# Optimization experiments

Hardware: AMD Instinct MI355X
Metric: run time of the kernel (lower is better)

The kernel has to match this reference:

```python
import jax, jax.numpy as jnp
import numpy as np

D_MODEL = 512
D_EMB = 300
D_FIXED = 30000
D_EXT = 32000
BS, L, J, N, T = 8, 256, 48, 32, 48


def setup_inputs() -> dict:
    key = jax.random.key(0)
    ks = jax.random.split(key, 32)
    s = 0.02
    def nrm(k, shape, scale=0.02):
        return jax.random.normal(k, shape, dtype=jnp.float32) * scale
    inp = {
        "Mp": jax.random.normal(ks[0], (BS, L, D_MODEL), dtype=jnp.float32),
        "Mq": jax.random.normal(ks[1], (BS, J, D_MODEL), dtype=jnp.float32),
        "Mqa": jax.random.normal(ks[2], (BS, N, D_MODEL), dtype=jnp.float32),
        "Mnlg": jax.random.normal(ks[3], (BS, T, D_MODEL), dtype=jnp.float32),
        "mask_p": jnp.ones((BS, L, 1), dtype=bool),
        "mask_q": jnp.ones((BS, J, 1), dtype=bool),
        "mask_qa": jnp.ones((BS, N, 1), dtype=bool),
        "source_ext": jax.random.randint(ks[4], (BS, L + J + N), 0, D_EXT, dtype=jnp.int64) if jax.config.jax_enable_x64 else jax.random.randint(ks[4], (BS, L + J + N), 0, D_EXT).astype(jnp.int32),
        "special_mask": jnp.ones((D_FIXED,), dtype=bool).at[jnp.array([0, 1, 2, 3])].set(False),
        "d_ext_vocab": D_EXT,
    }
    # additive attention params for question / qa / passage branches
    names = ["q", "a", "p"]
    for i, nme in enumerate(names):
        base = 5 + 5 * i
        inp[f"Wk_{nme}"] = nrm(ks[base + 0], (D_MODEL, D_MODEL))
        inp[f"bk_{nme}"] = jnp.zeros((D_MODEL,), dtype=jnp.float32)
        inp[f"Wq_{nme}"] = nrm(ks[base + 1], (D_MODEL, D_MODEL))
        inp[f"bq_{nme}"] = jnp.zeros((D_MODEL,), dtype=jnp.float32)
        inp[f"v_{nme}"] = nrm(ks[base + 2], (D_MODEL,))
    # vocab generator: Linear(d_model, d_emb) -> Linear(d_emb, d_fixed, bias=False)
    inp["W1"] = nrm(ks[20], (D_MODEL, D_EMB))
    inp["b1"] = jnp.zeros((D_EMB,), dtype=jnp.float32)
    inp["W2"] = nrm(ks[21], (D_EMB, D_FIXED))
    # mixture: Linear(4*d_model, 4) + softmax
    inp["Wm"] = nrm(ks[22], (4 * D_MODEL, 4))
    inp["bm"] = jnp.zeros((4,), dtype=jnp.float32)
    return inp


def _additive_attn(K, V, Q, mask, Wk, bk, Wq, bq, v):
    # K,V: [b,S,d]; Q: [b,T,d]; mask: [b,S,1] bool
    Kp = K @ Wk + bk                                  # [b,S,d]
    Qp = Q @ Wq + bq                                  # [b,T,d]
    scores = jnp.einsum("btsd,d->bts", jnp.tanh(Qp[:, :, None, :] + Kp[:, None, :, :]), v)
    scores = jnp.where(mask[:, None, :, 0], scores, -1e9)
    attn = jax.nn.softmax(scores, axis=-1)            # [b,T,S]
    ctx = jnp.einsum("bts,bsd->btd", attn, V)         # [b,T,d]
    return ctx, attn


def reference(Mp, Mq, Mqa, Mnlg, mask_p, mask_q, mask_qa, source_ext, special_mask,
              Wk_q, bk_q, Wq_q, bq_q, v_q,
              Wk_a, bk_a, Wq_a, bq_a, v_a,
              Wk_p, bk_p, Wq_p, bq_p, v_p,
              W1, b1, W2, Wm, bm, d_ext_vocab):
    d_fixed = special_mask.shape[0]
    bs, Tq, _ = Mnlg.shape

    ctx_q, q_distr = _additive_attn(Mq, Mq, Mnlg, mask_q, Wk_q, bk_q, Wq_q, bq_q, v_q)
    ctx_a, qa_distr = _additive_attn(Mqa, Mqa, Mnlg, mask_qa, Wk_a, bk_a, Wq_a, bq_a, v_a)
    ctx_p, p_distr = _additive_attn(Mp, Mp, Mnlg, mask_p, Wk_p, bk_p, Wq_p, bq_p, v_p)

    # fixed-vocab distribution with special tokens masked out
    logits = (Mnlg @ W1 + b1) @ W2                    # [b,T,d_fixed]
    logits = jnp.where(special_mask[None, None, :], logits, -1e9)
    fixed_vocab_distr = jax.nn.softmax(logits, axis=-1)

    # mixture weights
    mix_in = jnp.concatenate([Mnlg, ctx_q, ctx_a, ctx_p], axis=-1)  # [b,T,4d]
    lambdas = jax.nn.softmax(mix_in @ Wm + bm, axis=-1)             # [b,T,4]
    lam_v, lam_q, lam_qa, lam_p = jnp.split(lambdas, 4, axis=-1)

    fixed_vocab_distr = fixed_vocab_distr * lam_v
    source_distr = jnp.concatenate([p_distr * lam_p, q_distr * lam_q, qa_distr * lam_qa], axis=-1)  # [b,T,S_tot]

    # scatter-add over extended vocab (math-equivalent to one_hot + matmul)
    def _scatter(src, idx):
        # src: [T,S_tot], idx: [S_tot]
        return jnp.zeros((Tq, d_ext_vocab), src.dtype).at[:, idx].add(src)

    ext_vocab_distr = jax.vmap(_scatter)(source_distr, source_ext)  # [b,T,d_ext]
    ext_vocab_distr = ext_vocab_distr.at[:, :, :d_fixed].add(fixed_vocab_distr)
    return ext_vocab_distr, lambdas
```

## Files before the change

### kernel.cpp

```cpp
#include <hip/hip_runtime.h>
#include <math.h>

#define BS     8
#define LL     256
#define JJ     48
#define NN     32
#define TT     48
#define DM     512
#define DEMB   300
#define DFIX   30000
#define DEXT   32000
#define SRC_TOT (LL + JJ + NN)
#define ROWS   (BS * TT)
#define NT     235
#define KH     320

typedef float f32x4  __attribute__((ext_vector_type(4)));
typedef short bf16x8 __attribute__((ext_vector_type(8)));

__device__ __forceinline__ short f2bf(float f) {
    union { float f; unsigned u; } v; v.f = f;
    return (short)((v.u + 0x7FFFu + ((v.u >> 16) & 1u)) >> 16);
}
__device__ __forceinline__ float bf2f(short s) {
    union { unsigned u; float f; } v;
    v.u = ((unsigned)(unsigned short)s) << 16;
    return v.f;
}
__device__ __forceinline__ float fast_exp2(float x) {
#if __has_builtin(__builtin_amdgcn_exp2f)
    return __builtin_amdgcn_exp2f(x);
#else
    return exp2f(x);
#endif
}
__device__ __forceinline__ float fast_rcp(float x) {
#if __has_builtin(__builtin_amdgcn_rcpf)
    return __builtin_amdgcn_rcpf(x);
#else
    return 1.f / x;
#endif
}
__device__ __forceinline__ float fast_tanh(float x) {
    x = fminf(fmaxf(x, -15.f), 15.f);
    const float e = fast_exp2(x * 2.885390082f);
    return (e - 1.f) * fast_rcp(e + 1.f);
}
__device__ __forceinline__ bool smask_true(const void* smask, bool byteLayout, int i)
{
    if (byteLayout) return ((const unsigned char*)smask)[i] != 0;
    return ((const int*)smask)[i] != 0;
}
__device__ __forceinline__ void mask8(const void* smask, bool byteLayout, int i,
                                      int* mb)
{
    if (byteLayout) {
        const uchar4 a = ((const uchar4*)((const unsigned char*)smask + i))[0];
        const uchar4 b = ((const uchar4*)((const unsigned char*)smask + i))[1];
        mb[0]=a.x; mb[1]=a.y; mb[2]=a.z; mb[3]=a.w;
        mb[4]=b.x; mb[5]=b.y; mb[6]=b.z; mb[7]=b.w;
    } else {
        const int* p = (const int*)smask + i;
        #pragma unroll
        for (int j = 0; j < 8; ++j) mb[j] = p[j];
    }
}

struct PDesc { const float* src; short* dst; int K, N, Kp, ntx, tiles; };
struct PArgs { PDesc d[12]; int nd; };

__global__ __launch_bounds__(256) void prep_kernel(PArgs pa)
{
    __shared__ short T[64][72];
    int tile = blockIdx.x, g = 0;
    while (g + 1 < pa.nd && tile >= pa.d[g].tiles) { tile -= pa.d[g].tiles; ++g; }
    const PDesc d = pa.d[g];
    const int tid = threadIdx.x;

    if (d.ntx == 0) {
        const int i = (tile * 256 + tid) * 8;
        if (i < d.K) {
            const float4 a = ((const float4*)(d.src + i))[0];
            const float4 b = ((const float4*)(d.src + i))[1];
            bf16x8 v;
            v[0]=f2bf(a.x); v[1]=f2bf(a.y); v[2]=f2bf(a.z); v[3]=f2bf(a.w);
            v[4]=f2bf(b.x); v[5]=f2bf(b.y); v[6]=f2bf(b.z); v[7]=f2bf(b.w);
            *(bf16x8*)&d.dst[i] = v;
        }
        return;
    }

    const int kt = tile / d.ntx, nt = tile % d.ntx;
    const int k0 = kt * 64, n0 = nt * 64;
    {
        const int n = n0 + (tid & 63);
        #pragma unroll
        for (int p = 0; p < 16; ++p) {
            const int kk = p * 4 + (tid >> 6);
            const int k = k0 + kk;
            float v = 0.f;
            if (k < d.K && n < d.N) v = d.src[(size_t)k * d.N + n];
            T[kk][tid & 63] = f2bf(v);
        }
    }
    __syncthreads();
    {
        const int nn = tid >> 2;
        const int kq = (tid & 3) * 16;
        const int n = n0 + nn;
        if (n < d.N) {
            bf16x8 v0, v1;
            #pragma unroll
            for (int j = 0; j < 8; ++j) v0[j] = T[kq + j][nn];
            #pragma unroll
            for (int j = 0; j < 8; ++j) v1[j] = T[kq + 8 + j][nn];
            *(bf16x8*)&d.dst[(size_t)n * d.Kp + k0 + kq]     = v0;
            *(bf16x8*)&d.dst[(size_t)n * d.Kp + k0 + kq + 8] = v1;
        }
    }
}

struct GDesc { const short* A; const short* Bt; const float* bias; void* C;
               const void* smask; float* pstat;
               int M, N, K, Kp, nx, my, obf, npad, nt, tiles; };
struct GArgs { GDesc d[7]; int nd; };

__global__ __launch_bounds__(256) void gemm_bf16_kernel(GArgs ga)
{
    __shared__ short As[2][4][130][8];
    __shared__ short Bs[2][4][130][8];
    __shared__ float pm_s[128][2];
    __shared__ float ps_s[128][2];

    int tile = blockIdx.x, g = 0;
    while (g + 1 < ga.nd && tile >= ga.d[g].tiles) { tile -= ga.d[g].tiles; ++g; }
    const short* __restrict__ A  = ga.d[g].A;
    const short* __restrict__ Bt = ga.d[g].Bt;
    const float* bias = ga.d[g].bias;
    const int N = ga.d[g].N, Kp = ga.d[g].Kp;
    const int nx = ga.d[g].nx, my = ga.d[g].my, obf = ga.d[g].obf;
    const int npad = ga.d[g].npad;

    int bm, bn;
    if (my > 0) { bm = (tile % my) * 128; bn = (tile / my) * 128; }
    else        { bm = (tile / nx) * 128; bn = (tile % nx) * 128; }
    const int tid  = threadIdx.x;
    const int lane = tid & 63;
    const int wv   = tid >> 6;
    const int wm   = (wv >> 1) * 64;
    const int wn   = (wv & 1) * 64;

    bf16x8 ra[2], rb[2];

    auto loadA = [&](int k0) {
        #pragma unroll
        for (int p = 0; p < 2; ++p) {
            const int row = p * 64 + (tid >> 2);
            ra[p] = *(const bf16x8*)&A[(size_t)(bm + row) * Kp + k0 + (tid & 3) * 8];
        }
    };
    auto loadB = [&](int k0) {
        #pragma unroll
        for (int p = 0; p < 2; ++p) {
            const int idx = p * 256 + tid;
            const int n = idx >> 2, kb = idx & 3;
            const int gn = bn + n;
            bf16x8 v = {};
            if (gn < N) v = *(const bf16x8*)&Bt[(size_t)gn * Kp + k0 + kb * 8];
            rb[p] = v;
        }
    };
    auto storeA = [&](int buf) {
        const int kb = tid & 3;
        #pragma unroll
        for (int p = 0; p < 2; ++p)
            *(bf16x8*)&As[buf][kb][p * 64 + (tid >> 2)][0] = ra[p];
    };
    auto storeB = [&](int buf) {
        #pragma unroll
        for (int p = 0; p < 2; ++p) {
            const int idx = p * 256 + tid;
            const int n = idx >> 2, kb = idx & 3;
            *(bf16x8*)&Bs[buf][kb][n][0] = rb[p];
        }
    };

    f32x4 acc[4][4] = {};
    const int nk = Kp / 32;

    loadA(0); loadB(0);
    storeA(0); storeB(0);
    __syncthreads();

    for (int kk = 0; kk < nk; ++kk) {
        const int cur = kk & 1;
        if (kk + 1 < nk) { loadA((kk + 1) * 32); loadB((kk + 1) * 32); }
        bf16x8 af[4], bfr[4];
        #pragma unroll
        for (int i = 0; i < 4; ++i) {
            af[i]  = *(const bf16x8*)&As[cur][lane >> 4][wm + i * 16 + (lane & 15)][0];
            bfr[i] = *(const bf16x8*)&Bs[cur][lane >> 4][wn + i * 16 + (lane & 15)][0];
        }
        #pragma unroll
        for (int mi = 0; mi < 4; ++mi)
            #pragma unroll
            for (int ni = 0; ni < 4; ++ni)
                acc[mi][ni] = __builtin_amdgcn_mfma_f32_16x16x32_bf16(
                    af[mi], bfr[ni], acc[mi][ni], 0, 0, 0);
        if (kk + 1 < nk) { storeA(cur ^ 1); storeB(cur ^ 1); }
        __syncthreads();
    }

    if (obf == 0) {
        float* Cf = (float*)ga.d[g].C;
        #pragma unroll
        for (int ni = 0; ni < 4; ++ni) {
            const int gn = bn + wn + ni * 16 + (lane & 15);
            if (gn >= N) continue;
            const float bb = bias ? bias[gn] : 0.f;
            #pragma unroll
            for (int mi = 0; mi < 4; ++mi)
                #pragma unroll
                for (int r = 0; r < 4; ++r) {
                    const int gm = bm + wm + mi * 16 + (lane >> 4) * 4 + r;
                    Cf[(size_t)gm * N + gn] = acc[mi][ni][r] + bb;
                }
        }
    } else if (obf == 2) {
        short* Cs = (short*)ga.d[g].C;
        #pragma unroll
        for (int ni = 0; ni < 4; ++ni) {
            const int gn = bn + wn + ni * 16 + (lane & 15);
            if (gn >= npad) continue;
            const bool valid = (gn < N);
            const float bb = (valid && bias) ? bias[gn] : 0.f;
            #pragma unroll
            for (int mi = 0; mi < 4; ++mi)
                #pragma unroll
                for (int r = 0; r < 4; ++r) {
                    const int gm = bm + wm + mi * 16 + (lane >> 4) * 4 + r;
                    Cs[(size_t)gm * npad + gn] = valid ? f2bf(acc[mi][ni][r] + bb) : (short)0;
                }
        }
    } else {
        short* Cs = (short*)ga.d[g].C;
        const void* sm = ga.d[g].smask;
        const bool byteLayout = (((const int*)sm)[1] == 0x01010101);
        int mk[4];
        #pragma unroll
        for (int ni = 0; ni < 4; ++ni) {
            const int gn = bn + wn + ni * 16 + (lane & 15);
            const bool inb = (gn < N);
            mk[ni] = inb && smask_true(sm, byteLayout, inb ? gn : 0);
            if (inb) {
                #pragma unroll
                for (int mi = 0; mi < 4; ++mi)
                    #pragma unroll
                    for (int r = 0; r < 4; ++r) {
                        const int gm = bm + wm + mi * 16 + (lane >> 4) * 4 + r;
                        Cs[(size_t)gm * N + gn] = f2bf(acc[mi][ni][r]);
                    }
            }
        }
        #pragma unroll
        for (int mi = 0; mi < 4; ++mi) {
            #pragma unroll
            for (int r = 0; r < 4; ++r) {
                const int rl = wm + mi * 16 + (lane >> 4) * 4 + r;
                float vmax = -INFINITY;
                #pragma unroll
                for (int ni = 0; ni < 4; ++ni)
                    if (mk[ni]) vmax = fmaxf(vmax, acc[mi][ni][r]);
                #pragma unroll
                for (int o = 1; o < 16; o <<= 1)
                    vmax = fmaxf(vmax, __shfl_xor(vmax, o));
                float se = 0.f;
                #pragma unroll
                for (int ni = 0; ni < 4; ++ni)
                    if (mk[ni]) se += __expf(acc[mi][ni][r] - vmax);
                #pragma unroll
                for (int o = 1; o < 16; o <<= 1)
                    se += __shfl_xor(se, o);
                if ((lane & 15) == 0) {
                    pm_s[rl][wn >> 6] = vmax;
                    ps_s[rl][wn >> 6] = se;
                }
            }
        }
        __syncthreads();
        if (tid < 128) {
            const float mA = pm_s[tid][0], mB = pm_s[tid][1];
            const float sA = ps_s[tid][0], sB = ps_s[tid][1];
            const float m = fmaxf(mA, mB);
            float s = 0.f;
            if (sA > 0.f) s += sA * __expf(mA - m);
            if (sB > 0.f) s += sB * __expf(mB - m);
            float* ps = ga.d[g].pstat;
            const size_t idx = ((size_t)(bm + tid) * ga.d[g].nt + (bn >> 7)) * 2;
            ps[idx + 0] = m;
            ps[idx + 1] = s;
        }
    }
}

struct SDesc { const float* Kp; const float* Qp; const float* vv;
               int Sb, s0, cnt, off; };
struct SArgs { SDesc c[6]; };

__global__ __launch_bounds__(256) void scores_kernel(SArgs sa,
                                                     float* __restrict__ scb)
{
    const SDesc d = sa.c[blockIdx.y];
    const int bt   = blockIdx.x;
    const int b    = bt / TT;
    const int tid  = threadIdx.x;
    const int lane = tid & 63;
    const int wave = tid >> 6;

    float qp[8], vv[8];
    {
        const float4* q4 = (const float4*)(d.Qp + (size_t)bt * DM) + lane * 2;
        float4 a = q4[0], c = q4[1];
        qp[0]=a.x; qp[1]=a.y; qp[2]=a.z; qp[3]=a.w;
        qp[4]=c.x; qp[5]=c.y; qp[6]=c.z; qp[7]=c.w;
        const float4* v4 = (const float4*)d.vv + lane * 2;
        a = v4[0]; c = v4[1];
        vv[0]=a.x; vv[1]=a.y; vv[2]=a.z; vv[3]=a.w;
        vv[4]=c.x; vv[5]=c.y; vv[6]=c.z; vv[7]=c.w;
    }
    for (int s = wave; s < d.cnt; s += 4) {
        const float* krow = d.Kp + ((size_t)b * d.Sb + d.s0 + s) * DM + lane * 8;
        const float4 ka = ((const float4*)krow)[0];
        const float4 kb = ((const float4*)krow)[1];
        float acc = 0.f;
        acc = fmaf(vv[0], fast_tanh(qp[0] + ka.x), acc);
        acc = fmaf(vv[1], fast_tanh(qp[1] + ka.y), acc);
        acc = fmaf(vv[2], fast_tanh(qp[2] + ka.z), acc);
        acc = fmaf(vv[3], fast_tanh(qp[3] + ka.w), acc);
        acc = fmaf(vv[4], fast_tanh(qp[4] + kb.x), acc);
        acc = fmaf(vv[5], fast_tanh(qp[5] + kb.y), acc);
        acc = fmaf(vv[6], fast_tanh(qp[6] + kb.z), acc);
        acc = fmaf(vv[7], fast_tanh(qp[7] + kb.w), acc);
        #pragma unroll
        for (int off = 32; off; off >>= 1) acc += __shfl_xor(acc, off);
        if (lane == 0) scb[(size_t)bt * SRC_TOT + d.off + s] = acc;
    }
}

__global__ __launch_bounds__(512) void attn2mix_kernel(
    const float* __restrict__ scb,
    const short* __restrict__ Mqb, const short* __restrict__ Mqab,
    const short* __restrict__ Mpb, const float* __restrict__ Mnlg,
    const float* __restrict__ Wm, const float* __restrict__ bm,
    const float* __restrict__ pstat,
    float* __restrict__ dQ, float* __restrict__ dQA, float* __restrict__ dP,
    float* __restrict__ lam_ws, float* __restrict__ lam_out,
    float* __restrict__ stat)
{
    __shared__ float a_sh[SRC_TOT];
    __shared__ float cQ[DM], cA[DM], cP[DM];
    __shared__ float red[16];
    __shared__ float redm[32];
    __shared__ float s_lamv;
    const int bt   = blockIdx.x;
    const int b    = bt / TT;
    const int tid  = threadIdx.x;
    const int lane = tid & 63;
    const int wave = tid >> 6;
    const float* srow = scb + (size_t)bt * SRC_TOT;

    #pragma unroll
    for (int br = 0; br < 3; ++br) {
        const int off = (br == 0) ? 0 : (br == 1) ? JJ : (JJ + NN);
        const int cnt = (br == 0) ? JJ : (br == 1) ? NN : LL;
        float x = (tid < cnt) ? srow[off + tid] : -INFINITY;
        float m = x;
        #pragma unroll
        for (int o = 32; o; o >>= 1) m = fmaxf(m, __shfl_xor(m, o));
        if (lane == 0) red[wave] = m;
        __syncthreads();
        m = red[0];
        #pragma unroll
        for (int w = 1; w < 8; ++w) m = fmaxf(m, red[w]);
        float e = (tid < cnt) ? __expf(x - m) : 0.f;
        float ss = e;
        #pragma unroll
        for (int o = 32; o; o >>= 1) ss += __shfl_xor(ss, o);
        if (lane == 0) red[8 + wave] = ss;
        __syncthreads();
        float denom = 0.f;
        #pragma unroll
        for (int w = 0; w < 8; ++w) denom += red[8 + w];
        if (tid < cnt) {
            const float a = e / denom;
            a_sh[off + tid] = a;
            float* dst = (br == 0) ? dQ : (br == 1) ? dQA : dP;
            dst[(size_t)bt * cnt + tid] = a;
        }
        __syncthreads();
    }
    {
        float aQ = 0.f, aA = 0.f, aP = 0.f;
        for (int s = 0; s < JJ; ++s)
            aQ = fmaf(a_sh[s],           bf2f(Mqb [((size_t)b * JJ + s) * DM + tid]), aQ);
        for (int s = 0; s < NN; ++s)
            aA = fmaf(a_sh[JJ + s],      bf2f(Mqab[((size_t)b * NN + s) * DM + tid]), aA);
        for (int s = 0; s < LL; ++s)
            aP = fmaf(a_sh[JJ + NN + s], bf2f(Mpb [((size_t)b * LL + s) * DM + tid]), aP);
        cQ[tid] = aQ; cA[tid] = aA; cP[tid] = aP;
    }
    __syncthreads();
    {
        const float x0 = Mnlg[(size_t)bt * DM + tid];
        const float x1 = cQ[tid], x2 = cA[tid], x3 = cP[tid];
        const float4 w0 = *(const float4*)&Wm[(size_t)tid * 4];
        const float4 w1 = *(const float4*)&Wm[(size_t)(512 + tid) * 4];
        const float4 w2 = *(const float4*)&Wm[(size_t)(1024 + tid) * 4];
        const float4 w3 = *(const float4*)&Wm[(size_t)(1536 + tid) * 4];
        float acc[4];
        acc[0] = x0 * w0.x + x1 * w1.x + x2 * w2.x + x3 * w3.x;
        acc[1] = x0 * w0.y + x1 * w1.y + x2 * w2.y + x3 * w3.y;
        acc[2] = x0 * w0.z + x1 * w1.z + x2 * w2.z + x3 * w3.z;
        acc[3] = x0 * w0.w + x1 * w1.w + x2 * w2.w + x3 * w3.w;
        #pragma unroll
        for (int c = 0; c < 4; ++c)
            #pragma unroll
            for (int o = 32; o; o >>= 1) acc[c] += __shfl_xor(acc[c], o);
        if (lane == 0) {
            redm[wave * 4 + 0] = acc[0]; redm[wave * 4 + 1] = acc[1];
            redm[wave * 4 + 2] = acc[2]; redm[wave * 4 + 3] = acc[3];
        }
        __syncthreads();
        if (tid == 0) {
            float l[4];
            #pragma unroll
            for (int c = 0; c < 4; ++c) {
                float s = bm[c];
                #pragma unroll
                for (int w = 0; w < 8; ++w) s += redm[w * 4 + c];
                l[c] = s;
            }
            const float mx = fmaxf(fmaxf(l[0], l[1]), fmaxf(l[2], l[3]));
            const float e0 = __expf(l[0] - mx), e1 = __expf(l[1] - mx);
            const float e2 = __expf(l[2] - mx), e3 = __expf(l[3] - mx);
            const float inv = 1.f / (e0 + e1 + e2 + e3);
            s_lamv = e0 * inv;
            lam_ws[bt * 4 + 0] = e0 * inv; lam_out[bt * 4 + 0] = e0 * inv;
            lam_ws[bt * 4 + 1] = e1 * inv; lam_out[bt * 4 + 1] = e1 * inv;
            lam_ws[bt * 4 + 2] = e2 * inv; lam_out[bt * 4 + 2] = e2 * inv;
            lam_ws[bt * 4 + 3] = e3 * inv; lam_out[bt * 4 + 3] = e3 * inv;
        }
    }
    __syncthreads();
    if (wave == 0) {
        float m = -INFINITY;
        for (int c = lane; c < NT; c += 64)
            m = fmaxf(m, pstat[((size_t)bt * NT + c) * 2]);
        #pragma unroll
        for (int o = 32; o; o >>= 1) m = fmaxf(m, __shfl_xor(m, o));
        float s = 0.f;
        for (int c = lane; c < NT; c += 64) {
            const float pm = pstat[((size_t)bt * NT + c) * 2];
            const float ps = pstat[((size_t)bt * NT + c) * 2 + 1];
            if (ps > 0.f) s += ps * __expf(pm - m);
        }
        #pragma unroll
        for (int o = 32; o; o >>= 1) s += __shfl_xor(s, o);
        if (lane == 0) {
            stat[bt * 2 + 0] = m;
            stat[bt * 2 + 1] = s_lamv / s;
        }
    }
}

__global__ __launch_bounds__(1024) void writescatter_kernel(
    const short* __restrict__ logits, const void* __restrict__ smask,
    const float* __restrict__ stat, const float* __restrict__ lam,
    const float* __restrict__ dP, const float* __restrict__ dQ,
    const float* __restrict__ dQA, const void* __restrict__ src_ext,
    float* __restrict__ out)
{
    const bool byteLayout = (((const int*)smask)[1] == 0x01010101);
    const int r = blockIdx.x;
    const float m   = stat[r * 2 + 0];
    const float inv = stat[r * 2 + 1];

    const short* lrow = logits + (size_t)r * DFIX;
    float* orow = out + (size_t)r * DEXT;
    const int tid = threadIdx.x;
    #pragma unroll
    for (int k = 0; k < 4; ++k) {
        const int i = (k * 1024 + tid) * 8;
        if (i >= DEXT) continue;
        float4 o0 = make_float4(0.f, 0.f, 0.f, 0.f);
        float4 o1 = make_float4(0.f, 0.f, 0.f, 0.f);
        if (i < DFIX) {
            const bf16x8 v = *(const bf16x8*)&lrow[i];
            int mb[8]; mask8(smask, byteLayout, i, mb);
            o0.x = mb[0] ? __expf(bf2f(v[0]) - m) * inv : 0.f;
            o0.y = mb[1] ? __expf(bf2f(v[1]) - m) * inv : 0.f;
            o0.z = mb[2] ? __expf(bf2f(v[2]) - m) * inv : 0.f;
            o0.w = mb[3] ? __expf(bf2f(v[3]) - m) * inv : 0.f;
            o1.x = mb[4] ? __expf(bf2f(v[4]) - m) * inv : 0.f;
            o1.y = mb[5] ? __expf(bf2f(v[5]) - m) * inv : 0.f;
            o1.z = mb[6] ? __expf(bf2f(v[6]) - m) * inv : 0.f;
            o1.w = mb[7] ? __expf(bf2f(v[7]) - m) * inv : 0.f;
        }
        *(float4*)&orow[i]     = o0;
        *(float4*)&orow[i + 4] = o1;
    }
    __syncthreads();
    if (tid < SRC_TOT) {
        const int* s32 = (const int*)src_ext;
        const bool src64 = (s32[1] == 0 && s32[3] == 0 && s32[5] == 0 && s32[7] == 0);
        const int b = r / TT;
        const float lamq  = lam[r * 4 + 1];
        const float lamqa = lam[r * 4 + 2];
        const float lamp  = lam[r * 4 + 3];
        const int pos = b * SRC_TOT + tid;
        const int idx = src64 ? (int)((const long long*)src_ext)[pos] : s32[pos];
        float val;
        if      (tid < LL)      val = dP [(size_t)r * LL + tid]             * lamp;
        else if (tid < LL + JJ) val = dQ [(size_t)r * JJ + (tid - LL)]      * lamq;
        else                    val = dQA[(size_t)r * NN + (tid - LL - JJ)] * lamqa;
        atomicAdd(&orow[idx], val);
    }
}

extern "C" void kernel_launch(void* const* d_in, const int* in_sizes, int n_in,
                              void* d_out, int out_size, void* d_ws, size_t ws_size,
                              hipStream_t stream)
{
    const float* Mp   = (const float*)d_in[0];
    const float* Mq   = (const float*)d_in[1];
    const float* Mqa  = (const float*)d_in[2];
    const float* Mnlg = (const float*)d_in[3];
    const void* src_ext = d_in[7];
    const void* smask   = d_in[8];
    const float* Wk_q = (const float*)d_in[10];
    const float* bk_q = (const float*)d_in[11];
    const float* Wq_q = (const float*)d_in[12];
    const float* bq_q = (const float*)d_in[13];
    const float* v_q  = (const float*)d_in[14];
    const float* Wk_a = (const float*)d_in[15];
    const float* bk_a = (const float*)d_in[16];
    const float* Wq_a = (const float*)d_in[17];
    const float* bq_a = (const float*)d_in[18];
    const float* v_a  = (const float*)d_in[19];
    const float* Wk_p = (const float*)d_in[20];
    const float* bk_p = (const float*)d_in[21];
    const float* Wq_p = (const float*)d_in[22];
    const float* bq_p = (const float*)d_in[23];
    const float* v_p  = (const float*)d_in[24];
    const float* W1   = (const float*)d_in[25];
    const float* b1   = (const float*)d_in[26];
    const float* W2   = (const float*)d_in[27];
    const float* Wm   = (const float*)d_in[28];
    const float* bm   = (const float*)d_in[29];
    float* out = (float*)d_out;

    char* ws = (char*)d_ws;
    size_t off = 0;
    auto alloc = [&](size_t bytes) -> char* {
        char* p = ws + off;
        off += (bytes + 255) & ~(size_t)255;
        return p;
    };
    short* logits = (short*)alloc((size_t)ROWS * DFIX * 2);
    float* KpP    = (float*)alloc((size_t)BS * LL * DM * 4);
    float* KpQ    = (float*)alloc((size_t)BS * JJ * DM * 4);
    float* KpA    = (float*)alloc((size_t)BS * NN * DM * 4);
    float* QpQ    = (float*)alloc((size_t)ROWS * DM * 4);
    float* QpA    = (float*)alloc((size_t)ROWS * DM * 4);
    float* QpP    = (float*)alloc((size_t)ROWS * DM * 4);
    float* dP     = (float*)alloc((size_t)ROWS * LL * 4);
    float* dQ     = (float*)alloc((size_t)ROWS * JJ * 4);
    float* dQA    = (float*)alloc((size_t)ROWS * NN * 4);
    float* lam    = (float*)alloc((size_t)ROWS * 4 * 4);
    float* pstat  = (float*)alloc((size_t)ROWS * NT * 2 * 4);
    float* stat   = (float*)alloc((size_t)ROWS * 2 * 4);
    float* scb    = (float*)alloc((size_t)ROWS * SRC_TOT * 4);
    short* tWkq = (short*)alloc((size_t)DM * DM * 2);
    short* tWqq = (short*)alloc((size_t)DM * DM * 2);
    short* tWka = (short*)alloc((size_t)DM * DM * 2);
    short* tWqa = (short*)alloc((size_t)DM * DM * 2);
    short* tWkp = (short*)alloc((size_t)DM * DM * 2);
    short* tWqp = (short*)alloc((size_t)DM * DM * 2);
    short* tW1  = (short*)alloc((size_t)DEMB * DM * 2);
    short* tW2  = (short*)alloc((size_t)DFIX * KH * 2);
    short* Mp_bf   = (short*)alloc((size_t)BS * LL * DM * 2);
    short* Mq_bf   = (short*)alloc((size_t)BS * JJ * DM * 2);
    short* Mqa_bf  = (short*)alloc((size_t)BS * NN * DM * 2);
    short* Mnlg_bf = (short*)alloc((size_t)ROWS * DM * 2);
    short* Hh_bf   = (short*)alloc((size_t)ROWS * KH * 2);
    (void)ws_size; (void)in_sizes; (void)n_in; (void)out_size;

    PArgs pa;
    pa.nd = 12;
    pa.d[0]  = { Wk_p, tWkp, DM,   DM,   DM,  8,  64 };
    pa.d[1]  = { Wk_q, tWkq, DM,   DM,   DM,  8,  64 };
    pa.d[2]  = { Wk_a, tWka, DM,   DM,   DM,  8,  64 };
    pa.d[3]  = { Wq_q, tWqq, DM,   DM,   DM,  8,  64 };
    pa.d[4]  = { Wq_a, tWqa, DM,   DM,   DM,  8,  64 };
    pa.d[5]  = { Wq_p, tWqp, DM,   DM,   DM,  8,  64 };
    pa.d[6]  = { W1,   tW1,  DM,   DEMB, DM,  5,  40 };
    pa.d[7]  = { W2,   tW2,  DEMB, DFIX, KH,  469, 2345 };
    pa.d[8]  = { Mp,   Mp_bf,   BS*LL*DM, 0, 0, 0, (BS*LL*DM) / 2048 };
    pa.d[9]  = { Mq,   Mq_bf,   BS*JJ*DM, 0, 0, 0, (BS*JJ*DM) / 2048 };
    pa.d[10] = { Mqa,  Mqa_bf,  BS*NN*DM, 0, 0, 0, (BS*NN*DM) / 2048 };
    pa.d[11] = { Mnlg, Mnlg_bf, ROWS*DM,  0, 0, 0, (ROWS*DM) / 2048 };
    prep_kernel<<<64 * 6 + 40 + 2345 + 512 + 96 + 64 + 96, 256, 0, stream>>>(pa);

    GArgs gA;
    gA.nd = 1;
    gA.d[0] = { Mnlg_bf, tW1, b1, Hh_bf, nullptr, nullptr,
                ROWS, DEMB, DM, DM, 3, 0, 2, KH, 0, 9 };
    gemm_bf16_kernel<<<9, 256, 0, stream>>>(gA);

    GArgs gB;
    gB.nd = 7;
    gB.d[0] = { Mp_bf,   tWkp, bk_p,    KpP,    nullptr, nullptr,
                BS*LL, DM,   DM,   DM,  4,   0, 0, DM,   0,  64 };
    gB.d[1] = { Mq_bf,   tWkq, bk_q,    KpQ,    nullptr, nullptr,
                BS*JJ, DM,   DM,   DM,  4,   0, 0, DM,   0,  12 };
    gB.d[2] = { Mqa_bf,  tWka, bk_a,    KpA,    nullptr, nullptr,
                BS*NN, DM,   DM,   DM,  4,   0, 0, DM,   0,   8 };
    gB.d[3] = { Mnlg_bf, tWqq, bq_q,    QpQ,    nullptr, nullptr,
                ROWS,  DM,   DM,   DM,  4,   0, 0, DM,   0,  12 };
    gB.d[4] = { Mnlg_bf, tWqa, bq_a,    QpA,    nullptr, nullptr,
                ROWS,  DM,   DM,   DM,  4,   0, 0, DM,   0,  12 };
    gB.d[5] = { Mnlg_bf, tWqp, bq_p,    QpP,    nullptr, nullptr,
                ROWS,  DM,   DM,   DM,  4,   0, 0, DM,   0,  12 };
    gB.d[6] = { Hh_bf,   tW2,  nullptr, logits, smask,   pstat,
                ROWS,  DFIX, DEMB, KH,  235, 3, 1, DFIX, NT, 705 };
    gemm_bf16_kernel<<<825, 256, 0, stream>>>(gB);

    SArgs sa;
    sa.c[0] = { KpQ, QpQ, v_q, JJ,   0, JJ,  0 };
    sa.c[1] = { KpA, QpA, v_a, NN,   0, NN,  JJ };
    sa.c[2] = { KpP, QpP, v_p, LL,   0, 64,  JJ + NN };
    sa.c[3] = { KpP, QpP, v_p, LL,  64, 64,  JJ + NN + 64 };
    sa.c[4] = { KpP, QpP, v_p, LL, 128, 64,  JJ + NN + 128 };
    sa.c[5] = { KpP, QpP, v_p, LL, 192, 64,  JJ + NN + 192 };
    scores_kernel<<<dim3(ROWS, 6), 256, 0, stream>>>(sa, scb);
    attn2mix_kernel<<<ROWS, 512, 0, stream>>>(scb, Mq_bf, Mqa_bf, Mp_bf, Mnlg,
                                              Wm, bm, pstat, dQ, dQA, dP, lam,
                                              out + (size_t)ROWS * DEXT, stat);

    writescatter_kernel<<<ROWS, 1024, 0, stream>>>(
        logits, smask, stat, lam, dP, dQ, dQA, src_ext, out);
}
```

Before: 157.2 us.

## Restructure launch schedule into fused stage kernels with bf16 projection outputs

Reorganizes the six-launch pipeline into four. W2 transposition now runs alongside the small projection GEMMs, and the large vocab GEMM shares a launch with the attention-score computation. The K/Q projections are stored in bf16 instead of fp32, which halves their traffic in the scores stage. The mixture kernel is merged with the final softmax write and scatter, so attention weights and lambdas stay in shared memory instead of round-tripping through global buffers. The cost is extra bf16 rounding on projections and heterogeneous blocks sharing a union of shared memory.

```diff
diff --git a/kernel.cpp b/kernel.cpp
--- a/kernel.cpp
+++ b/kernel.cpp
@@ -66,17 +66,23 @@
     }
 }
 
+struct SmemGemm {
+    short As[2][4][130][8];
+    short Bs[2][4][130][8];
+    float pm[128][2];
+    float ps[128][2];
+};
+union SmemU {
+    SmemGemm g;
+    short T[64][72];
+};
+
 struct PDesc { const float* src; short* dst; int K, N, Kp, ntx, tiles; };
-struct PArgs { PDesc d[12]; int nd; };
-
-__global__ __launch_bounds__(256) void prep_kernel(PArgs pa)
-{
-    __shared__ short T[64][72];
-    int tile = blockIdx.x, g = 0;
-    while (g + 1 < pa.nd && tile >= pa.d[g].tiles) { tile -= pa.d[g].tiles; ++g; }
-    const PDesc d = pa.d[g];
+struct PArgs { PDesc d[11]; int nd; };
+
+__device__ __forceinline__ void dev_prep(const PDesc& d, int tile, short (*T)[72])
+{
     const int tid = threadIdx.x;
-
     if (d.ntx == 0) {
         const int i = (tile * 256 + tid) * 8;
         if (i < d.K) {
@@ -89,7 +95,6 @@
         }
         return;
     }
-
     const int kt = tile / d.ntx, nt = tile % d.ntx;
     const int k0 = kt * 64, n0 = nt * 64;
     {
@@ -120,26 +125,27 @@
     }
 }
 
+__global__ __launch_bounds__(256) void prep_kernel(PArgs pa)
+{
+    __shared__ short T[64][72];
+    int tile = blockIdx.x, g = 0;
+    while (g + 1 < pa.nd && tile >= pa.d[g].tiles) { tile -= pa.d[g].tiles; ++g; }
+    dev_prep(pa.d[g], tile, T);
+}
+
 struct GDesc { const short* A; const short* Bt; const float* bias; void* C;
                const void* smask; float* pstat;
                int M, N, K, Kp, nx, my, obf, npad, nt, tiles; };
 struct GArgs { GDesc d[7]; int nd; };
 
-__global__ __launch_bounds__(256) void gemm_bf16_kernel(GArgs ga)
-{
-    __shared__ short As[2][4][130][8];
-    __shared__ short Bs[2][4][130][8];
-    __shared__ float pm_s[128][2];
-    __shared__ float ps_s[128][2];
-
-    int tile = blockIdx.x, g = 0;
-    while (g + 1 < ga.nd && tile >= ga.d[g].tiles) { tile -= ga.d[g].tiles; ++g; }
-    const short* __restrict__ A  = ga.d[g].A;
-    const short* __restrict__ Bt = ga.d[g].Bt;
-    const float* bias = ga.d[g].bias;
-    const int N = ga.d[g].N, Kp = ga.d[g].Kp;
-    const int nx = ga.d[g].nx, my = ga.d[g].my, obf = ga.d[g].obf;
-    const int npad = ga.d[g].npad;
+__device__ void dev_gemm(const GDesc& d, int tile, SmemGemm& sm)
+{
+    const short* __restrict__ A  = d.A;
+    const short* __restrict__ Bt = d.Bt;
+    const float* bias = d.bias;
+    const int N = d.N, Kp = d.Kp;
+    const int nx = d.nx, my = d.my, obf = d.obf;
+    const int npad = d.npad;
 
     int bm, bn;
     if (my > 0) { bm = (tile % my) * 128; bn = (tile / my) * 128; }
@@ -174,14 +180,14 @@
         const int kb = tid & 3;
         #pragma unroll
         for (int p = 0; p < 2; ++p)
-            *(bf16x8*)&As[buf][kb][p * 64 + (tid >> 2)][0] = ra[p];
+            *(bf16x8*)&sm.As[buf][kb][p * 64 + (tid >> 2)][0] = ra[p];
     };
     auto storeB = [&](int buf) {
         #pragma unroll
         for (int p = 0; p < 2; ++p) {
             const int idx = p * 256 + tid;
             const int n = idx >> 2, kb = idx & 3;
-            *(bf16x8*)&Bs[buf][kb][n][0] = rb[p];
+            *(bf16x8*)&sm.Bs[buf][kb][n][0] = rb[p];
         }
     };
 
@@ -198,8 +204,8 @@
         bf16x8 af[4], bfr[4];
         #pragma unroll
         for (int i = 0; i < 4; ++i) {
-            af[i]  = *(const bf16x8*)&As[cur][lane >> 4][wm + i * 16 + (lane & 15)][0];
-            bfr[i] = *(const bf16x8*)&Bs[cur][lane >> 4][wn + i * 16 + (lane & 15)][0];
+            af[i]  = *(const bf16x8*)&sm.As[cur][lane >> 4][wm + i * 16 + (lane & 15)][0];
+            bfr[i] = *(const bf16x8*)&sm.Bs[cur][lane >> 4][wn + i * 16 + (lane & 15)][0];
         }
         #pragma unroll
         for (int mi = 0; mi < 4; ++mi)
@@ -212,7 +218,7 @@
     }
 
     if (obf == 0) {
-        float* Cf = (float*)ga.d[g].C;
+        float* Cf = (float*)d.C;
         #pragma unroll
         for (int ni = 0; ni < 4; ++ni) {
             const int gn = bn + wn + ni * 16 + (lane & 15);
@@ -227,7 +233,7 @@
                 }
         }
     } else if (obf == 2) {
-        short* Cs = (short*)ga.d[g].C;
+        short* Cs = (short*)d.C;
         #pragma unroll
         for (int ni = 0; ni < 4; ++ni) {
             const int gn = bn + wn + ni * 16 + (lane & 15);
@@ -243,15 +249,15 @@
                 }
         }
     } else {
-        short* Cs = (short*)ga.d[g].C;
-        const void* sm = ga.d[g].smask;
-        const bool byteLayout = (((const int*)sm)[1] == 0x01010101);
+        short* Cs = (short*)d.C;
+        const void* sm2 = d.smask;
+        const bool byteLayout = (((const int*)sm2)[1] == 0x01010101);
         int mk[4];
         #pragma unroll
         for (int ni = 0; ni < 4; ++ni) {
             const int gn = bn + wn + ni * 16 + (lane & 15);
             const bool inb = (gn < N);
-            mk[ni] = inb && smask_true(sm, byteLayout, inb ? gn : 0);
+            mk[ni] = inb && smask_true(sm2, byteLayout, inb ? gn : 0);
             if (inb) {
                 #pragma unroll
                 for (int mi = 0; mi < 4; ++mi)
@@ -282,36 +288,33 @@
                 for (int o = 1; o < 16; o <<= 1)
                     se += __shfl_xor(se, o);
                 if ((lane & 15) == 0) {
-                    pm_s[rl][wn >> 6] = vmax;
-                    ps_s[rl][wn >> 6] = se;
+                    sm.pm[rl][wn >> 6] = vmax;
+                    sm.ps[rl][wn >> 6] = se;
                 }
             }
         }
         __syncthreads();
         if (tid < 128) {
-            const float mA = pm_s[tid][0], mB = pm_s[tid][1];
-            const float sA = ps_s[tid][0], sB = ps_s[tid][1];
+            const float mA = sm.pm[tid][0], mB = sm.pm[tid][1];
+            const float sA = sm.ps[tid][0], sB = sm.ps[tid][1];
             const float m = fmaxf(mA, mB);
             float s = 0.f;
             if (sA > 0.f) s += sA * __expf(mA - m);
             if (sB > 0.f) s += sB * __expf(mB - m);
-            float* ps = ga.d[g].pstat;
-            const size_t idx = ((size_t)(bm + tid) * ga.d[g].nt + (bn >> 7)) * 2;
+            float* ps = d.pstat;
+            const size_t idx = ((size_t)(bm + tid) * d.nt + (bn >> 7)) * 2;
             ps[idx + 0] = m;
             ps[idx + 1] = s;
         }
     }
 }
 
-struct SDesc { const float* Kp; const float* Qp; const float* vv;
+struct SDesc { const short* Kp; const short* Qp; const float* vv;
                int Sb, s0, cnt, off; };
 struct SArgs { SDesc c[6]; };
 
-__global__ __launch_bounds__(256) void scores_kernel(SArgs sa,
-                                                     float* __restrict__ scb)
-{
-    const SDesc d = sa.c[blockIdx.y];
-    const int bt   = blockIdx.x;
+__device__ void dev_scores(const SDesc& d, int bt, float* __restrict__ scb)
+{
     const int b    = bt / TT;
     const int tid  = threadIdx.x;
     const int lane = tid & 63;
@@ -319,49 +322,70 @@
 
     float qp[8], vv[8];
     {
-        const float4* q4 = (const float4*)(d.Qp + (size_t)bt * DM) + lane * 2;
-        float4 a = q4[0], c = q4[1];
-        qp[0]=a.x; qp[1]=a.y; qp[2]=a.z; qp[3]=a.w;
-        qp[4]=c.x; qp[5]=c.y; qp[6]=c.z; qp[7]=c.w;
-        const float4* v4 = (const float4*)d.vv + lane * 2;
-        a = v4[0]; c = v4[1];
+        const bf16x8 q = *(const bf16x8*)&d.Qp[(size_t)bt * DM + lane * 8];
+        #pragma unroll
+        for (int j = 0; j < 8; ++j) qp[j] = bf2f(q[j]);
+        const float4 a = ((const float4*)(d.vv + lane * 8))[0];
+        const float4 c = ((const float4*)(d.vv + lane * 8))[1];
         vv[0]=a.x; vv[1]=a.y; vv[2]=a.z; vv[3]=a.w;
         vv[4]=c.x; vv[5]=c.y; vv[6]=c.z; vv[7]=c.w;
     }
     for (int s = wave; s < d.cnt; s += 4) {
-        const float* krow = d.Kp + ((size_t)b * d.Sb + d.s0 + s) * DM + lane * 8;
-        const float4 ka = ((const float4*)krow)[0];
-        const float4 kb = ((const float4*)krow)[1];
+        const bf16x8 kv = *(const bf16x8*)&d.Kp[((size_t)b * d.Sb + d.s0 + s) * DM + lane * 8];
         float acc = 0.f;
-        acc = fmaf(vv[0], fast_tanh(qp[0] + ka.x), acc);
-        acc = fmaf(vv[1], fast_tanh(qp[1] + ka.y), acc);
-        acc = fmaf(vv[2], fast_tanh(qp[2] + ka.z), acc);
-        acc = fmaf(vv[3], fast_tanh(qp[3] + ka.w), acc);
-        acc = fmaf(vv[4], fast_tanh(qp[4] + kb.x), acc);
-        acc = fmaf(vv[5], fast_tanh(qp[5] + kb.y), acc);
-        acc = fmaf(vv[6], fast_tanh(qp[6] + kb.z), acc);
-        acc = fmaf(vv[7], fast_tanh(qp[7] + kb.w), acc);
+        #pragma unroll
+        for (int j = 0; j < 8; ++j)
+            acc = fmaf(vv[j], fast_tanh(qp[j] + bf2f(kv[j])), acc);
         #pragma unroll
         for (int off = 32; off; off >>= 1) acc += __shfl_xor(acc, off);
         if (lane == 0) scb[(size_t)bt * SRC_TOT + d.off + s] = acc;
     }
 }
 
-__global__ __launch_bounds__(512) void attn2mix_kernel(
+__global__ __launch_bounds__(256) void l2_kernel(PArgs pa, GArgs ga)
+{
+    __shared__ SmemU u;
+    int tile = blockIdx.x;
+    if (tile < pa.d[0].tiles) {
+        dev_prep(pa.d[0], tile, u.T);
+        return;
+    }
+    tile -= pa.d[0].tiles;
+    int g = 0;
+    while (g + 1 < ga.nd && tile >= ga.d[g].tiles) { tile -= ga.d[g].tiles; ++g; }
+    dev_gemm(ga.d[g], tile, u.g);
+}
+
+__global__ __launch_bounds__(256) void l3_kernel(GArgs ga, SArgs sa,
+                                                 float* __restrict__ scb)
+{
+    __shared__ SmemU u;
+    if ((int)blockIdx.x < ga.d[0].tiles) {
+        dev_gemm(ga.d[0], blockIdx.x, u.g);
+        return;
+    }
+    const int idx = blockIdx.x - ga.d[0].tiles;
+    const int bt  = idx % ROWS;
+    const int ch  = idx / ROWS;
+    dev_scores(sa.c[ch], bt, scb);
+}
+
+__global__ __launch_bounds__(512) void finale_kernel(
     const float* __restrict__ scb,
     const short* __restrict__ Mqb, const short* __restrict__ Mqab,
     const short* __restrict__ Mpb, const float* __restrict__ Mnlg,
     const float* __restrict__ Wm, const float* __restrict__ bm,
     const float* __restrict__ pstat,
-    float* __restrict__ dQ, float* __restrict__ dQA, float* __restrict__ dP,
-    float* __restrict__ lam_ws, float* __restrict__ lam_out,
-    float* __restrict__ stat)
+    const short* __restrict__ logits, const void* __restrict__ smask,
+    const void* __restrict__ src_ext,
+    float* __restrict__ out, float* __restrict__ lam_out)
 {
     __shared__ float a_sh[SRC_TOT];
     __shared__ float cQ[DM], cA[DM], cP[DM];
     __shared__ float red[16];
     __shared__ float redm[32];
-    __shared__ float s_lamv;
+    __shared__ float s_lam[4];
+    __shared__ float s_stat[2];
     const int bt   = blockIdx.x;
     const int b    = bt / TT;
     const int tid  = threadIdx.x;
@@ -391,20 +415,18 @@
         float denom = 0.f;
         #pragma unroll
         for (int w = 0; w < 8; ++w) denom += red[8 + w];
-        if (tid < cnt) {
-            const float a = e / denom;
-            a_sh[off + tid] = a;
-            float* dst = (br == 0) ? dQ : (br == 1) ? dQA : dP;
-            dst[(size_t)bt * cnt + tid] = a;
-        }
+        if (tid < cnt) a_sh[off + tid] = e / denom;
         __syncthreads();
     }
     {
         float aQ = 0.f, aA = 0.f, aP = 0.f;
+        #pragma unroll 4
         for (int s = 0; s < JJ; ++s)
             aQ = fmaf(a_sh[s],           bf2f(Mqb [((size_t)b * JJ + s) * DM + tid]), aQ);
+        #pragma unroll 4
         for (int s = 0; s < NN; ++s)
             aA = fmaf(a_sh[JJ + s],      bf2f(Mqab[((size_t)b * NN + s) * DM + tid]), aA);
+        #pragma unroll 4
         for (int s = 0; s < LL; ++s)
             aP = fmaf(a_sh[JJ + NN + s], bf2f(Mpb [((size_t)b * LL + s) * DM + tid]), aP);
         cQ[tid] = aQ; cA[tid] = aA; cP[tid] = aP;
@@ -444,11 +466,10 @@
             const float e0 = __expf(l[0] - mx), e1 = __expf(l[1] - mx);
             const float e2 = __expf(l[2] - mx), e3 = __expf(l[3] - mx);
             const float inv = 1.f / (e0 + e1 + e2 + e3);
-            s_lamv = e0 * inv;
-            lam_ws[bt * 4 + 0] = e0 * inv; lam_out[bt * 4 + 0] = e0 * inv;
-            lam_ws[bt * 4 + 1] = e1 * inv; lam_out[bt * 4 + 1] = e1 * inv;
-            lam_ws[bt * 4 + 2] = e2 * inv; lam_out[bt * 4 + 2] = e2 * inv;
-            lam_ws[bt * 4 + 3] = e3 * inv; lam_out[bt * 4 + 3] = e3 * inv;
+            s_lam[0] = e0 * inv; s_lam[1] = e1 * inv;
+            s_lam[2] = e2 * inv; s_lam[3] = e3 * inv;
+            lam_out[bt * 4 + 0] = e0 * inv; lam_out[bt * 4 + 1] = e1 * inv;
+            lam_out[bt * 4 + 2] = e2 * inv; lam_out[bt * 4 + 3] = e3 * inv;
         }
     }
     __syncthreads();
@@ -466,64 +487,48 @@
         }
         #pragma unroll
         for (int o = 32; o; o >>= 1) s += __shfl_xor(s, o);
-        if (lane == 0) {
-            stat[bt * 2 + 0] = m;
-            stat[bt * 2 + 1] = s_lamv / s;
-        }
-    }
-}
-
-__global__ __launch_bounds__(1024) void writescatter_kernel(
-    const short* __restrict__ logits, const void* __restrict__ smask,
-    const float* __restrict__ stat, const float* __restrict__ lam,
-    const float* __restrict__ dP, const float* __restrict__ dQ,
-    const float* __restrict__ dQA, const void* __restrict__ src_ext,
-    float* __restrict__ out)
-{
-    const bool byteLayout = (((const int*)smask)[1] == 0x01010101);
-    const int r = blockIdx.x;
-    const float m   = stat[r * 2 + 0];
-    const float inv = stat[r * 2 + 1];
-
-    const short* lrow = logits + (size_t)r * DFIX;
-    float* orow = out + (size_t)r * DEXT;
-    const int tid = threadIdx.x;
-    #pragma unroll
-    for (int k = 0; k < 4; ++k) {
-        const int i = (k * 1024 + tid) * 8;
-        if (i >= DEXT) continue;
-        float4 o0 = make_float4(0.f, 0.f, 0.f, 0.f);
-        float4 o1 = make_float4(0.f, 0.f, 0.f, 0.f);
-        if (i < DFIX) {
-            const bf16x8 v = *(const bf16x8*)&lrow[i];
-            int mb[8]; mask8(smask, byteLayout, i, mb);
-            o0.x = mb[0] ? __expf(bf2f(v[0]) - m) * inv : 0.f;
-            o0.y = mb[1] ? __expf(bf2f(v[1]) - m) * inv : 0.f;
-            o0.z = mb[2] ? __expf(bf2f(v[2]) - m) * inv : 0.f;
-            o0.w = mb[3] ? __expf(bf2f(v[3]) - m) * inv : 0.f;
-            o1.x = mb[4] ? __expf(bf2f(v[4]) - m) * inv : 0.f;
-            o1.y = mb[5] ? __expf(bf2f(v[5]) - m) * inv : 0.f;
-            o1.z = mb[6] ? __expf(bf2f(v[6]) - m) * inv : 0.f;
-            o1.w = mb[7] ? __expf(bf2f(v[7]) - m) * inv : 0.f;
-        }
-        *(float4*)&orow[i]     = o0;
-        *(float4*)&orow[i + 4] = o1;
+        if (lane == 0) { s_stat[0] = m; s_stat[1] = s_lam[0] / s; }
+    }
+    __syncthreads();
+    {
+        const bool byteLayout = (((const int*)smask)[1] == 0x01010101);
+        const float m   = s_stat[0];
+        const float inv = s_stat[1];
+        const short* lrow = logits + (size_t)bt * DFIX;
+        float* orow = out + (size_t)bt * DEXT;
+        #pragma unroll
+        for (int k = 0; k < 8; ++k) {
+            const int i = (k * 512 + tid) * 8;
+            if (i >= DEXT) continue;
+            float4 o0 = make_float4(0.f, 0.f, 0.f, 0.f);
+            float4 o1 = make_float4(0.f, 0.f, 0.f, 0.f);
+            if (i < DFIX) {
+                const bf16x8 v = *(const bf16x8*)&lrow[i];
+                int mb[8]; mask8(smask, byteLayout, i, mb);
+                o0.x = mb[0] ? __expf(bf2f(v[0]) - m) * inv : 0.f;
+                o0.y = mb[1] ? __expf(bf2f(v[1]) - m) * inv : 0.f;
+                o0.z = mb[2] ? __expf(bf2f(v[2]) - m) * inv : 0.f;
+                o0.w = mb[3] ? __expf(bf2f(v[3]) - m) * inv : 0.f;
+                o1.x = mb[4] ? __expf(bf2f(v[4]) - m) * inv : 0.f;
+                o1.y = mb[5] ? __expf(bf2f(v[5]) - m) * inv : 0.f;
+                o1.z = mb[6] ? __expf(bf2f(v[6]) - m) * inv : 0.f;
+                o1.w = mb[7] ? __expf(bf2f(v[7]) - m) * inv : 0.f;
+            }
+            *(float4*)&orow[i]     = o0;
+            *(float4*)&orow[i + 4] = o1;
+        }
     }
     __syncthreads();
     if (tid < SRC_TOT) {
         const int* s32 = (const int*)src_ext;
         const bool src64 = (s32[1] == 0 && s32[3] == 0 && s32[5] == 0 && s32[7] == 0);
-        const int b = r / TT;
-        const float lamq  = lam[r * 4 + 1];
-        const float lamqa = lam[r * 4 + 2];
-        const float lamp  = lam[r * 4 + 3];
         const int pos = b * SRC_TOT + tid;
         const int idx = src64 ? (int)((const long long*)src_ext)[pos] : s32[pos];
         float val;
-        if      (tid < LL)      val = dP [(size_t)r * LL + tid]             * lamp;
-        else if (tid < LL + JJ) val = dQ [(size_t)r * JJ + (tid - LL)]      * lamq;
-        else                    val = dQA[(size_t)r * NN + (tid - LL - JJ)] * lamqa;
-        atomicAdd(&orow[idx], val);
+        if      (tid < LL)      val = a_sh[JJ + NN + tid]   * s_lam[3];
+        else if (tid < LL + JJ) val = a_sh[tid - LL]        * s_lam[1];
+        else                    val = a_sh[JJ + (tid - LL - JJ)] * s_lam[2];
+        atomicAdd(&out[(size_t)bt * DEXT + idx], val);
     }
 }
 
@@ -567,18 +572,13 @@
         return p;
     };
     short* logits = (short*)alloc((size_t)ROWS * DFIX * 2);
-    float* KpP    = (float*)alloc((size_t)BS * LL * DM * 4);
-    float* KpQ    = (float*)alloc((size_t)BS * JJ * DM * 4);
-    float* KpA    = (float*)alloc((size_t)BS * NN * DM * 4);
-    float* QpQ    = (float*)alloc((size_t)ROWS * DM * 4);
-    float* QpA    = (float*)alloc((size_t)ROWS * DM * 4);
-    float* QpP    = (float*)alloc((size_t)ROWS * DM * 4);
-    float* dP     = (float*)alloc((size_t)ROWS * LL * 4);
-    float* dQ     = (float*)alloc((size_t)ROWS * JJ * 4);
-    float* dQA    = (float*)alloc((size_t)ROWS * NN * 4);
-    float* lam    = (float*)alloc((size_t)ROWS * 4 * 4);
+    short* KpP    = (short*)alloc((size_t)BS * LL * DM * 2);
+    short* KpQ    = (short*)alloc((size_t)BS * JJ * DM * 2);
+    short* KpA    = (short*)alloc((size_t)BS * NN * DM * 2);
+    short* QpQ    = (short*)alloc((size_t)ROWS * DM * 2);
+    short* QpA    = (short*)alloc((size_t)ROWS * DM * 2);
+    short* QpP    = (short*)alloc((size_t)ROWS * DM * 2);
     float* pstat  = (float*)alloc((size_t)ROWS * NT * 2 * 4);
-    float* stat   = (float*)alloc((size_t)ROWS * 2 * 4);
     float* scb    = (float*)alloc((size_t)ROWS * SRC_TOT * 4);
     short* tWkq = (short*)alloc((size_t)DM * DM * 2);
     short* tWqq = (short*)alloc((size_t)DM * DM * 2);
@@ -595,46 +595,46 @@
     short* Hh_bf   = (short*)alloc((size_t)ROWS * KH * 2);
     (void)ws_size; (void)in_sizes; (void)n_in; (void)out_size;
 
-    PArgs pa;
-    pa.nd = 12;
-    pa.d[0]  = { Wk_p, tWkp, DM,   DM,   DM,  8,  64 };
-    pa.d[1]  = { Wk_q, tWkq, DM,   DM,   DM,  8,  64 };
-    pa.d[2]  = { Wk_a, tWka, DM,   DM,   DM,  8,  64 };
-    pa.d[3]  = { Wq_q, tWqq, DM,   DM,   DM,  8,  64 };
-    pa.d[4]  = { Wq_a, tWqa, DM,   DM,   DM,  8,  64 };
-    pa.d[5]  = { Wq_p, tWqp, DM,   DM,   DM,  8,  64 };
-    pa.d[6]  = { W1,   tW1,  DM,   DEMB, DM,  5,  40 };
-    pa.d[7]  = { W2,   tW2,  DEMB, DFIX, KH,  469, 2345 };
-    pa.d[8]  = { Mp,   Mp_bf,   BS*LL*DM, 0, 0, 0, (BS*LL*DM) / 2048 };
-    pa.d[9]  = { Mq,   Mq_bf,   BS*JJ*DM, 0, 0, 0, (BS*JJ*DM) / 2048 };
-    pa.d[10] = { Mqa,  Mqa_bf,  BS*NN*DM, 0, 0, 0, (BS*NN*DM) / 2048 };
-    pa.d[11] = { Mnlg, Mnlg_bf, ROWS*DM,  0, 0, 0, (ROWS*DM) / 2048 };
-    prep_kernel<<<64 * 6 + 40 + 2345 + 512 + 96 + 64 + 96, 256, 0, stream>>>(pa);
-
-    GArgs gA;
-    gA.nd = 1;
-    gA.d[0] = { Mnlg_bf, tW1, b1, Hh_bf, nullptr, nullptr,
-                ROWS, DEMB, DM, DM, 3, 0, 2, KH, 0, 9 };
-    gemm_bf16_kernel<<<9, 256, 0, stream>>>(gA);
-
-    GArgs gB;
-    gB.nd = 7;
-    gB.d[0] = { Mp_bf,   tWkp, bk_p,    KpP,    nullptr, nullptr,
-                BS*LL, DM,   DM,   DM,  4,   0, 0, DM,   0,  64 };
-    gB.d[1] = { Mq_bf,   tWkq, bk_q,    KpQ,    nullptr, nullptr,
-                BS*JJ, DM,   DM,   DM,  4,   0, 0, DM,   0,  12 };
-    gB.d[2] = { Mqa_bf,  tWka, bk_a,    KpA,    nullptr, nullptr,
-                BS*NN, DM,   DM,   DM,  4,   0, 0, DM,   0,   8 };
-    gB.d[3] = { Mnlg_bf, tWqq, bq_q,    QpQ,    nullptr, nullptr,
-                ROWS,  DM,   DM,   DM,  4,   0, 0, DM,   0,  12 };
-    gB.d[4] = { Mnlg_bf, tWqa, bq_a,    QpA,    nullptr, nullptr,
-                ROWS,  DM,   DM,   DM,  4,   0, 0, DM,   0,  12 };
-    gB.d[5] = { Mnlg_bf, tWqp, bq_p,    QpP,    nullptr, nullptr,
-                ROWS,  DM,   DM,   DM,  4,   0, 0, DM,   0,  12 };
-    gB.d[6] = { Hh_bf,   tW2,  nullptr, logits, smask,   pstat,
-                ROWS,  DFIX, DEMB, KH,  235, 3, 1, DFIX, NT, 705 };
-    gemm_bf16_kernel<<<825, 256, 0, stream>>>(gB);
-
+    PArgs p1;
+    p1.nd = 11;
+    p1.d[0]  = { Wk_p, tWkp, DM, DM,   DM, 8, 64 };
+    p1.d[1]  = { Wk_q, tWkq, DM, DM,   DM, 8, 64 };
+    p1.d[2]  = { Wk_a, tWka, DM, DM,   DM, 8, 64 };
+    p1.d[3]  = { Wq_q, tWqq, DM, DM,   DM, 8, 64 };
+    p1.d[4]  = { Wq_a, tWqa, DM, DM,   DM, 8, 64 };
+    p1.d[5]  = { Wq_p, tWqp, DM, DM,   DM, 8, 64 };
+    p1.d[6]  = { W1,   tW1,  DM, DEMB, DM, 5, 40 };
+    p1.d[7]  = { Mp,   Mp_bf,   BS*LL*DM, 0, 0, 0, (BS*LL*DM) / 2048 };
+    p1.d[8]  = { Mq,   Mq_bf,   BS*JJ*DM, 0, 0, 0, (BS*JJ*DM) / 2048 };
+    p1.d[9]  = { Mqa,  Mqa_bf,  BS*NN*DM, 0, 0, 0, (BS*NN*DM) / 2048 };
+    p1.d[10] = { Mnlg, Mnlg_bf, ROWS*DM,  0, 0, 0, (ROWS*DM) / 2048 };
+    prep_kernel<<<64 * 6 + 40 + 512 + 96 + 64 + 96, 256, 0, stream>>>(p1);
+
+    PArgs p2;
+    p2.nd = 1;
+    p2.d[0] = { W2, tW2, DEMB, DFIX, KH, 469, 2345 };
+    GArgs g2;
+    g2.nd = 7;
+    g2.d[0] = { Mnlg_bf, tW1,  b1,   Hh_bf, nullptr, nullptr,
+                ROWS,  DEMB, DM, DM, 3, 0, 2, KH, 0,  9 };
+    g2.d[1] = { Mp_bf,   tWkp, bk_p, KpP,   nullptr, nullptr,
+                BS*LL, DM,   DM, DM, 4, 0, 2, DM, 0, 64 };
+    g2.d[2] = { Mq_bf,   tWkq, bk_q, KpQ,   nullptr, nullptr,
+                BS*JJ, DM,   DM, DM, 4, 0, 2, DM, 0, 12 };
+    g2.d[3] = { Mqa_bf,  tWka, bk_a, KpA,   nullptr, nullptr,
+                BS*NN, DM,   DM, DM, 4, 0, 2, DM, 0,  8 };
+    g2.d[4] = { Mnlg_bf, tWqq, bq_q, QpQ,   nullptr, nullptr,
+                ROWS,  DM,   DM, DM, 4, 0, 2, DM, 0, 12 };
+    g2.d[5] = { Mnlg_bf, tWqa, bq_a, QpA,   nullptr, nullptr,
+                ROWS,  DM,   DM, DM, 4, 0, 2, DM, 0, 12 };
+    g2.d[6] = { Mnlg_bf, tWqp, bq_p, QpP,   nullptr, nullptr,
+                ROWS,  DM,   DM, DM, 4, 0, 2, DM, 0, 12 };
+    l2_kernel<<<2345 + 129, 256, 0, stream>>>(p2, g2);
+
+    GArgs g3;
+    g3.nd = 1;
+    g3.d[0] = { Hh_bf, tW2, nullptr, logits, smask, pstat,
+                ROWS, DFIX, DEMB, KH, 235, 3, 1, DFIX, NT, 705 };
     SArgs sa;
     sa.c[0] = { KpQ, QpQ, v_q, JJ,   0, JJ,  0 };
     sa.c[1] = { KpA, QpA, v_a, NN,   0, NN,  JJ };
@@ -642,11 +642,9 @@
     sa.c[3] = { KpP, QpP, v_p, LL,  64, 64,  JJ + NN + 64 };
     sa.c[4] = { KpP, QpP, v_p, LL, 128, 64,  JJ + NN + 128 };
     sa.c[5] = { KpP, QpP, v_p, LL, 192, 64,  JJ + NN + 192 };
-    scores_kernel<<<dim3(ROWS, 6), 256, 0, stream>>>(sa, scb);
-    attn2mix_kernel<<<ROWS, 512, 0, stream>>>(scb, Mq_bf, Mqa_bf, Mp_bf, Mnlg,
-                                              Wm, bm, pstat, dQ, dQA, dP, lam,
-                                              out + (size_t)ROWS * DEXT, stat);
-
-    writescatter_kernel<<<ROWS, 1024, 0, stream>>>(
-        logits, smask, stat, lam, dP, dQ, dQA, src_ext, out);
-}
+    l3_kernel<<<705 + 6 * ROWS, 256, 0, stream>>>(g3, sa, scb);
+
+    finale_kernel<<<ROWS, 512, 0, stream>>>(
+        scb, Mq_bf, Mqa_bf, Mp_bf, Mnlg, Wm, bm, pstat,
+        logits, smask, src_ext, out, out + (size_t)ROWS * DEXT);
+}
```

Measured after the change: 171.1 us. 8.8% more time.
